# Kernel tuning notes

Hardware: AMD Instinct MI355X
Metric: run time of the kernel (lower is better)

## Reference

```python
import jax, jax.numpy as jnp
import numpy as np

HEADS, POINTS = 8, 4
EPS = 1e-5
BS, C, H, W = 2, 256, 200, 200


def _layernorm(x, g, b):
    m = x.mean(-1, keepdims=True)
    v = ((x - m) ** 2).mean(-1, keepdims=True)
    return (x - m) / jnp.sqrt(v + EPS) * g + b


def _sine_pos(bs, Hh, Ww, num_feats, temperature=10000.0):
    # mmdet SinePositionalEncoding with all-zeros mask: cumsum of ones -> 1..H / 1..W
    y = jnp.arange(1, Hh + 1, dtype=jnp.float32)
    x = jnp.arange(1, Ww + 1, dtype=jnp.float32)
    dim_t = jnp.arange(num_feats, dtype=jnp.float32)
    dim_t = temperature ** (2.0 * jnp.floor(dim_t / 2.0) / num_feats)

    def interleave(p):  # p: [N, num_feats] -> [sin(p0),cos(p1),sin(p2),...]
        return jnp.stack((jnp.sin(p[:, 0::2]), jnp.cos(p[:, 1::2])), axis=-1).reshape(p.shape[0], -1)

    pos_x = interleave(x[:, None] / dim_t)  # [W, nf]
    pos_y = interleave(y[:, None] / dim_t)  # [H, nf]
    pos = jnp.concatenate([
        jnp.broadcast_to(pos_y[:, None, :], (Hh, Ww, num_feats)),
        jnp.broadcast_to(pos_x[None, :, :], (Hh, Ww, num_feats)),
    ], axis=-1)  # [H, W, 2*nf] (channel order matches cat((pos_y,pos_x),dim=1) after flatten/permute)
    return jnp.broadcast_to(pos.reshape(1, Hh * Ww, 2 * num_feats), (bs, Hh * Ww, 2 * num_feats))


def _bilinear_sample(v, x, y):
    # v: [bs, heads, H, W, hd]; x, y: [bs, heads, N] pixel coords (align_corners=False, zero padding)
    bs, nh, Hh, Ww, hd = v.shape
    vf = v.reshape(bs, nh, Hh * Ww, hd)
    x0 = jnp.floor(x)
    y0 = jnp.floor(y)
    wx = x - x0
    wy = y - y0

    def gather(xi, yi):
        valid = (xi >= 0) & (xi < Ww) & (yi >= 0) & (yi < Hh)
        xc = jnp.clip(xi, 0, Ww - 1).astype(jnp.int32)
        yc = jnp.clip(yi, 0, Hh - 1).astype(jnp.int32)
        idx = yc * Ww + xc
        g = jnp.take_along_axis(vf, idx[..., None], axis=2)  # [bs, nh, N, hd]
        return g * valid[..., None].astype(v.dtype)

    out = gather(x0, y0) * ((1 - wx) * (1 - wy))[..., None]
    out = out + gather(x0 + 1, y0) * (wx * (1 - wy))[..., None]
    out = out + gather(x0, y0 + 1) * ((1 - wx) * wy)[..., None]
    out = out + gather(x0 + 1, y0 + 1) * (wx * wy)[..., None]
    return out


def _dfa_layer(out, ref, pos, Hh, Ww, p):
    bs, Lq, Cc = out.shape
    hd = Cc // HEADS
    q = out + pos
    value = out @ p['vp_w'].T + p['vp_b']  # [bs, Lq, C]
    off = (q @ p['off_w'].T + p['off_b']).reshape(bs, Lq, HEADS, POINTS, 2)
    aw = jax.nn.softmax((q @ p['aw_w'].T + p['aw_b']).reshape(bs, Lq, HEADS, POINTS), axis=-1)
    norm = jnp.array([Ww, Hh], dtype=out.dtype)
    loc = ref[None, :, None, None, :] + off / norm  # [bs, Lq, heads, P, 2] normalized [0,1]
    x = loc[..., 0] * Ww - 0.5
    y = loc[..., 1] * Hh - 0.5
    v = value.reshape(bs, Lq, HEADS, hd).transpose(0, 2, 1, 3).reshape(bs, HEADS, Hh, Ww, hd)
    xt = x.transpose(0, 2, 1, 3).reshape(bs, HEADS, Lq * POINTS)
    yt = y.transpose(0, 2, 1, 3).reshape(bs, HEADS, Lq * POINTS)
    samp = _bilinear_sample(v, xt, yt).reshape(bs, HEADS, Lq, POINTS, hd)
    attn = jnp.einsum('bhqpd,bqhp->bqhd', samp, aw).reshape(bs, Lq, Cc)
    attn = attn @ p['op_w'].T + p['op_b']
    out = _layernorm(out + attn, p['ln1_g'], p['ln1_b'])
    ffn = jax.nn.relu(out @ p['l1_w'].T + p['l1_b']) @ p['l2_w'].T + p['l2_b']
    return _layernorm(out + ffn, p['ln2_g'], p['ln2_b'])


def setup_inputs() -> dict:
    key = jax.random.key(0)
    ks = jax.random.split(key, 20)
    s = 0.02
    L = 3
    return {
        'bev_feat': jax.random.normal(ks[0], (BS, C, H, W), jnp.float32),
        'proj_q_w': jax.random.normal(ks[1], (C, C), jnp.float32) * s,
        'proj_q_b': jax.random.normal(ks[2], (C,), jnp.float32) * s,
        'off_w': jax.random.normal(ks[3], (L, HEADS * POINTS * 2, C), jnp.float32) * s,
        'off_b': jax.random.normal(ks[4], (L, HEADS * POINTS * 2), jnp.float32) * s,
        'aw_w': jax.random.normal(ks[5], (L, HEADS * POINTS, C), jnp.float32) * s,
        'aw_b': jax.random.normal(ks[6], (L, HEADS * POINTS), jnp.float32) * s,
        'vp_w': jax.random.normal(ks[7], (L, C, C), jnp.float32) * s,
        'vp_b': jax.random.normal(ks[8], (L, C), jnp.float32) * s,
        'op_w': jax.random.normal(ks[9], (L, C, C), jnp.float32) * s,
        'op_b': jax.random.normal(ks[10], (L, C), jnp.float32) * s,
        'ln1_g': jnp.ones((L, C), jnp.float32),
        'ln1_b': jnp.zeros((L, C), jnp.float32),
        'l1_w': jax.random.normal(ks[11], (L, C, C), jnp.float32) * s,
        'l1_b': jax.random.normal(ks[12], (L, C), jnp.float32) * s,
        'l2_w': jax.random.normal(ks[13], (L, C, C), jnp.float32) * s,
        'l2_b': jax.random.normal(ks[14], (L, C), jnp.float32) * s,
        'ln2_g': jnp.ones((L, C), jnp.float32),
        'ln2_b': jnp.zeros((L, C), jnp.float32),
    }


def reference(bev_feat, proj_q_w, proj_q_b, off_w, off_b, aw_w, aw_b, vp_w, vp_b,
              op_w, op_b, ln1_g, ln1_b, l1_w, l1_b, l2_w, l2_b, ln2_g, ln2_b):
    bs, Cc, Hh, Ww = bev_feat.shape
    x = bev_feat.reshape(bs, Cc, Hh * Ww).transpose(0, 2, 1)  # [bs, HW, C]
    out = x @ proj_q_w.T + proj_q_b
    # reference points: pixel centers normalized to [0,1]
    ry, rx = jnp.meshgrid(jnp.linspace(0.5, Hh - 0.5, Hh) / Hh,
                          jnp.linspace(0.5, Ww - 0.5, Ww) / Ww, indexing='ij')
    ref = jnp.stack([rx.reshape(-1), ry.reshape(-1)], axis=-1).astype(bev_feat.dtype)  # [HW, 2]
    pos = _sine_pos(bs, Hh, Ww, Cc // 2).astype(bev_feat.dtype)
    n_layers = off_w.shape[0]
    for i in range(n_layers):
        p = dict(off_w=off_w[i], off_b=off_b[i], aw_w=aw_w[i], aw_b=aw_b[i],
                 vp_w=vp_w[i], vp_b=vp_b[i], op_w=op_w[i], op_b=op_b[i],
                 ln1_g=ln1_g[i], ln1_b=ln1_b[i], l1_w=l1_w[i], l1_b=l1_b[i],
                 l2_w=l2_w[i], l2_b=l2_b[i], ln2_g=ln2_g[i], ln2_b=ln2_b[i])
        out = _dfa_layer(out, ref, pos, Hh, Ww, p)
    return out.transpose(0, 2, 1).reshape(bs, Cc, Hh, Ww)
```

## Files before the change

### kernel.cpp

```cpp
#include <hip/hip_runtime.h>
#include <math.h>

#define HEADS 8
#define POINTS 4
#define BSZ 2
#define CDIM 256
#define HH 200
#define WW 200
#define LQ (HH * WW)
#define MTOT (BSZ * LQ)
#define NLAYERS 3

typedef __attribute__((ext_vector_type(8))) short shortx8;
typedef __attribute__((ext_vector_type(4))) float floatx4;

__device__ __forceinline__ ushort f2b(float f) {
    union { float f; unsigned u; } v; v.f = f;
    unsigned r = v.u + 0x7fffu + ((v.u >> 16) & 1u);
    return (ushort)(r >> 16);
}
__device__ __forceinline__ float b2f(ushort b) {
    union { unsigned u; float f; } v; v.u = ((unsigned)b) << 16;
    return v.f;
}
__device__ __forceinline__ float bitsf(unsigned u) {
    union { unsigned u; float f; } v; v.u = u;
    return v.f;
}

__global__ __launch_bounds__(256)
void cvt_kernel(const float* __restrict__ in, ushort* __restrict__ out)
{
    const int i = (blockIdx.x * 256 + threadIdx.x) * 4;
    const float4 v = *(const float4*)(in + i);
    ushort4 o;
    o.x = f2b(v.x); o.y = f2b(v.y); o.z = f2b(v.z); o.w = f2b(v.w);
    *(ushort4*)(out + i) = o;
}

__global__ __launch_bounds__(256)
void build_offaw(const float* __restrict__ offw, const float* __restrict__ offb,
                 const float* __restrict__ aww, const float* __restrict__ awb,
                 ushort* __restrict__ wout, float* __restrict__ bout)
{
    const int blk = blockIdx.x;
    const int i = blk >> 7;
    const int r = blk & 127;
    const int c = threadIdx.x;
    float v = 0.f;
    if (r < 64)      v = offw[((size_t)i * 64 + r) * CDIM + c];
    else if (r < 96) v = aww[((size_t)i * 32 + (r - 64)) * CDIM + c];
    wout[((size_t)i * 128 + r) * CDIM + c] = f2b(v);
    if (c == 0) {
        float bb = 0.f;
        if (r < 64)      bb = offb[i * 64 + r];
        else if (r < 96) bb = awb[i * 32 + (r - 64)];
        bout[i * 128 + r] = bb;
    }
}

__global__ __launch_bounds__(256)
void pos_kernel(ushort* __restrict__ pos)
{
    const int idx = blockIdx.x * 256 + threadIdx.x;
    const int c = idx & 255;
    const int l = idx >> 8;
    const int cc = c & 127;
    const float coord = (c < 128) ? (float)(l / WW + 1) : (float)(l % WW + 1);
    const float expo = (float)(2 * (cc >> 1)) * (1.0f / 128.0f);
    const float t = powf(10000.0f, expo);
    const float ph = coord / t;
    pos[idx] = f2b((cc & 1) ? cosf(ph) : sinf(ph));
}

__global__ __launch_bounds__(256)
void bevT_kernel(const float* __restrict__ in, ushort* __restrict__ out)
{
    __shared__ float tile[32][33];
    const int b = blockIdx.z;
    const int l0 = blockIdx.x * 32;
    const int c0 = blockIdx.y * 32;
    const float* ib = in + (size_t)b * CDIM * LQ;
    ushort* ob = out + (size_t)b * LQ * CDIM;
    #pragma unroll
    for (int j = 0; j < 32; j += 8)
        tile[threadIdx.y + j][threadIdx.x] =
            ib[(size_t)(c0 + threadIdx.y + j) * LQ + l0 + threadIdx.x];
    __syncthreads();
    #pragma unroll
    for (int j = 0; j < 32; j += 8)
        ob[(size_t)(l0 + threadIdx.y + j) * CDIM + c0 + threadIdx.x] =
            f2b(tile[threadIdx.x][threadIdx.y + j]);
}

#define LSTR 40

template<bool RELU, bool F32OUT, bool BF16OUT, bool QOUT>
__global__ __launch_bounds__(256)
void mfma_gemm(const ushort* __restrict__ A, const ushort* __restrict__ B,
               const float* __restrict__ bias,
               float* __restrict__ Cf, ushort* __restrict__ Cb,
               ushort* __restrict__ Cq, const ushort* __restrict__ posb,
               int N, int K)
{
    __shared__ ushort As[128 * LSTR];
    __shared__ ushort Bs[128 * LSTR];
    const int tid = threadIdx.x;
    const int lane = tid & 63;
    const int wave = tid >> 6;
    const int wr = (wave >> 1) * 64;
    const int wc = (wave & 1) * 64;
    const int rowBase = blockIdx.y * 128;
    const int colBase = blockIdx.x * 128;

    floatx4 acc[4][4];
    #pragma unroll
    for (int i = 0; i < 4; i++)
        #pragma unroll
        for (int j = 0; j < 4; j++) {
            floatx4 z = {0.f, 0.f, 0.f, 0.f};
            acc[i][j] = z;
        }

    const int strow = tid >> 2;
    const int stcol = (tid & 3) * 8;
    const int kq = (lane >> 4) * 8;
    const int lr = lane & 15;

    for (int k0 = 0; k0 < K; k0 += 32) {
        #pragma unroll
        for (int j = 0; j < 2; j++) {
            const int r = j * 64 + strow;
            const uint4 av = *(const uint4*)(A + (size_t)(rowBase + r) * K + k0 + stcol);
            const uint4 bv = *(const uint4*)(B + (size_t)(colBase + r) * K + k0 + stcol);
            *(uint4*)(As + r * LSTR + stcol) = av;
            *(uint4*)(Bs + r * LSTR + stcol) = bv;
        }
        __syncthreads();
        shortx8 af[4], bf[4];
        #pragma unroll
        for (int t = 0; t < 4; t++) {
            af[t] = *(const shortx8*)(As + (wr + t * 16 + lr) * LSTR + kq);
            bf[t] = *(const shortx8*)(Bs + (wc + t * 16 + lr) * LSTR + kq);
        }
        #pragma unroll
        for (int mt = 0; mt < 4; mt++)
            #pragma unroll
            for (int nt = 0; nt < 4; nt++)
                acc[mt][nt] = __builtin_amdgcn_mfma_f32_16x16x32_bf16(
                    af[mt], bf[nt], acc[mt][nt], 0, 0, 0);
        __syncthreads();
    }

    const int colB = colBase + wc + lr;
    const int rowB = rowBase + wr + (lane >> 4) * 4;
    #pragma unroll
    for (int mt = 0; mt < 4; mt++) {
        #pragma unroll
        for (int r = 0; r < 4; r++) {
            const int m = rowB + mt * 16 + r;
            const int pr = (m >= LQ) ? m - LQ : m;
            #pragma unroll
            for (int nt = 0; nt < 4; nt++) {
                const int n = colB + nt * 16;
                float v = acc[mt][nt][r] + bias[n];
                if (RELU) v = fmaxf(v, 0.f);
                if (F32OUT) Cf[(size_t)m * N + n] = v;
                if (BF16OUT) Cb[(size_t)m * N + n] = f2b(v);
                if (QOUT) {
                    const float pv = b2f(posb[(size_t)pr * CDIM + n]);
                    Cq[(size_t)m * N + n] = f2b(v + pv);
                }
            }
        }
    }
}

__global__ __launch_bounds__(256)
void sample_kernel(const ushort* __restrict__ val,
                   const float* __restrict__ offaw,
                   ushort* __restrict__ attn)
{
    const int wave = threadIdx.x >> 6;
    const int lane = threadIdx.x & 63;
    const int m = blockIdx.x * 4 + wave;
    const int b = (m >= LQ) ? 1 : 0;
    const int l = m - b * LQ;
    const int head = lane >> 3;
    const int c = head * 32 + (lane & 7) * 4;

    const float* row = offaw + (size_t)m * 128;
    const float4 lg  = *(const float4*)(row + 64 + head * 4);
    const float4 o01 = *(const float4*)(row + head * 8);
    const float4 o23 = *(const float4*)(row + head * 8 + 4);

    const float mx = fmaxf(fmaxf(lg.x, lg.y), fmaxf(lg.z, lg.w));
    const float e0 = expf(lg.x - mx), e1 = expf(lg.y - mx);
    const float e2 = expf(lg.z - mx), e3 = expf(lg.w - mx);
    const float inv = 1.0f / (e0 + e1 + e2 + e3);
    const float awv[4] = {e0 * inv, e1 * inv, e2 * inv, e3 * inv};

    const float lx = (float)(l % WW);
    const float ly = (float)(l / WW);
    const float px[4] = {lx + o01.x, lx + o01.z, lx + o23.x, lx + o23.z};
    const float py[4] = {ly + o01.y, ly + o01.w, ly + o23.y, ly + o23.w};

    const ushort* vb = val + (size_t)b * LQ * CDIM;
    uint2 cv[16];
    float cw[16];
    #pragma unroll
    for (int p = 0; p < POINTS; p++) {
        const float x = px[p], y = py[p];
        const float xf = floorf(x), yf = floorf(y);
        const int x0 = (int)xf, y0 = (int)yf;
        const float wx = x - xf, wy = y - yf;
        const int x0c = min(max(x0, 0), WW - 1);
        const int x1c = min(max(x0 + 1, 0), WW - 1);
        const int y0c = min(max(y0, 0), HH - 1);
        const int y1c = min(max(y0 + 1, 0), HH - 1);
        const float vx0 = (x0 >= 0 && x0 < WW) ? 1.f : 0.f;
        const float vx1 = (x0 + 1 >= 0 && x0 + 1 < WW) ? 1.f : 0.f;
        const float vy0 = (y0 >= 0 && y0 < HH) ? 1.f : 0.f;
        const float vy1 = (y0 + 1 >= 0 && y0 + 1 < HH) ? 1.f : 0.f;
        const float a = awv[p];
        cw[p * 4 + 0] = a * (1.f - wx) * (1.f - wy) * vx0 * vy0;
        cw[p * 4 + 1] = a * wx * (1.f - wy) * vx1 * vy0;
        cw[p * 4 + 2] = a * (1.f - wx) * wy * vx0 * vy1;
        cw[p * 4 + 3] = a * wx * wy * vx1 * vy1;
        const int r0 = y0c * WW, r1 = y1c * WW;
        cv[p * 4 + 0] = *(const uint2*)(vb + (size_t)(r0 + x0c) * CDIM + c);
        cv[p * 4 + 1] = *(const uint2*)(vb + (size_t)(r0 + x1c) * CDIM + c);
        cv[p * 4 + 2] = *(const uint2*)(vb + (size_t)(r1 + x0c) * CDIM + c);
        cv[p * 4 + 3] = *(const uint2*)(vb + (size_t)(r1 + x1c) * CDIM + c);
    }
    float a0 = 0.f, a1 = 0.f, a2 = 0.f, a3 = 0.f;
    #pragma unroll
    for (int i = 0; i < 16; i++) {
        const float wgt = cw[i];
        a0 = fmaf(wgt, bitsf(cv[i].x << 16), a0);
        a1 = fmaf(wgt, bitsf(cv[i].x & 0xffff0000u), a1);
        a2 = fmaf(wgt, bitsf(cv[i].y << 16), a2);
        a3 = fmaf(wgt, bitsf(cv[i].y & 0xffff0000u), a3);
    }
    ushort4 o;
    o.x = f2b(a0); o.y = f2b(a1); o.z = f2b(a2); o.w = f2b(a3);
    *(ushort4*)(attn + (size_t)m * CDIM + c) = o;
}

__global__ __launch_bounds__(256)
void ln_kernel(float* __restrict__ io, const ushort* __restrict__ add,
               const float* __restrict__ g, const float* __restrict__ beta,
               ushort* __restrict__ outb, ushort* __restrict__ qout,
               const ushort* __restrict__ posb)
{
    const int row = blockIdx.x * 4 + (threadIdx.x >> 6);
    const int lane = threadIdx.x & 63;
    float4* rp = (float4*)(io + (size_t)row * CDIM);
    float4 x = rp[lane];
    const ushort4 av = *(const ushort4*)(add + (size_t)row * CDIM + lane * 4);
    x.x += b2f(av.x); x.y += b2f(av.y); x.z += b2f(av.z); x.w += b2f(av.w);
    float s = x.x + x.y + x.z + x.w;
    float sq = x.x * x.x + x.y * x.y + x.z * x.z + x.w * x.w;
    #pragma unroll
    for (int o = 32; o >= 1; o >>= 1) {
        s += __shfl_xor(s, o, 64);
        sq += __shfl_xor(sq, o, 64);
    }
    const float mean = s * (1.0f / CDIM);
    const float var = sq * (1.0f / CDIM) - mean * mean;
    const float rstd = rsqrtf(var + 1e-5f);
    const float4 gv = *(const float4*)(g + lane * 4);
    const float4 bv = *(const float4*)(beta + lane * 4);
    float4 o4;
    o4.x = (x.x - mean) * rstd * gv.x + bv.x;
    o4.y = (x.y - mean) * rstd * gv.y + bv.y;
    o4.z = (x.z - mean) * rstd * gv.z + bv.z;
    o4.w = (x.w - mean) * rstd * gv.w + bv.w;
    rp[lane] = o4;
    ushort4 ob;
    ob.x = f2b(o4.x); ob.y = f2b(o4.y); ob.z = f2b(o4.z); ob.w = f2b(o4.w);
    *(ushort4*)(outb + (size_t)row * CDIM + lane * 4) = ob;
    if (qout) {
        const int pr = (row >= LQ) ? row - LQ : row;
        const ushort4 pp = *(const ushort4*)(posb + (size_t)pr * CDIM + lane * 4);
        ushort4 qq;
        qq.x = f2b(o4.x + b2f(pp.x)); qq.y = f2b(o4.y + b2f(pp.y));
        qq.z = f2b(o4.z + b2f(pp.z)); qq.w = f2b(o4.w + b2f(pp.w));
        *(ushort4*)(qout + (size_t)row * CDIM + lane * 4) = qq;
    }
}

__global__ __launch_bounds__(256)
void transpose_out(const float* __restrict__ in, float* __restrict__ outp)
{
    __shared__ float tile[32][33];
    const int b = blockIdx.z;
    const int l0 = blockIdx.x * 32;
    const int c0 = blockIdx.y * 32;
    const float* ib = in + (size_t)b * LQ * CDIM;
    float* ob = outp + (size_t)b * CDIM * LQ;
    #pragma unroll
    for (int j = 0; j < 32; j += 8)
        tile[threadIdx.y + j][threadIdx.x] =
            ib[(size_t)(l0 + threadIdx.y + j) * CDIM + c0 + threadIdx.x];
    __syncthreads();
    #pragma unroll
    for (int j = 0; j < 32; j += 8)
        ob[(size_t)(c0 + threadIdx.y + j) * LQ + l0 + threadIdx.x] =
            tile[threadIdx.x][threadIdx.y + j];
}

extern "C" void kernel_launch(void* const* d_in, const int* in_sizes, int n_in,
                              void* d_out, int out_size, void* d_ws, size_t ws_size,
                              hipStream_t stream)
{
    const float* bev      = (const float*)d_in[0];
    const float* proj_q_w = (const float*)d_in[1];
    const float* proj_q_b = (const float*)d_in[2];
    const float* off_w    = (const float*)d_in[3];
    const float* off_b    = (const float*)d_in[4];
    const float* aw_w     = (const float*)d_in[5];
    const float* aw_b     = (const float*)d_in[6];
    const float* vp_w     = (const float*)d_in[7];
    const float* vp_b     = (const float*)d_in[8];
    const float* op_w     = (const float*)d_in[9];
    const float* op_b     = (const float*)d_in[10];
    const float* ln1_g    = (const float*)d_in[11];
    const float* ln1_b    = (const float*)d_in[12];
    const float* l1_w     = (const float*)d_in[13];
    const float* l1_b     = (const float*)d_in[14];
    const float* l2_w     = (const float*)d_in[15];
    const float* l2_b     = (const float*)d_in[16];
    const float* ln2_g    = (const float*)d_in[17];
    const float* ln2_b    = (const float*)d_in[18];
    float* outp = (float*)d_out;

    char* w = (char*)d_ws;
    float*  out_f   = (float*)(w);
    float*  offaw_f = (float*)(w + 81920000);
    ushort* tmp_b   = (ushort*)(w + 122880000);
    ushort* out_b   = (ushort*)(w + 163840000);
    ushort* q_b     = (ushort*)(w + 204800000);
    ushort* val_b   = (ushort*)(w + 245760000);
    ushort* pos_b   = (ushort*)(w + 286720000);
    ushort* w_b     = (ushort*)(w + 307200000);
    ushort* wproj = w_b;
    ushort* wvp   = w_b + 65536;
    ushort* wop   = w_b + 65536 + 196608;
    ushort* wl1   = w_b + 65536 + 2 * 196608;
    ushort* wl2   = w_b + 65536 + 3 * 196608;
    ushort* wofa  = w_b + 65536 + 4 * 196608;
    float*  bofa  = (float*)(w + 307200000 + 2 * (65536 + 4 * 196608 + 98304));

    const dim3 blk(256);

    cvt_kernel<<<dim3(65536 / 1024), blk, 0, stream>>>(proj_q_w, wproj);
    cvt_kernel<<<dim3(196608 / 1024), blk, 0, stream>>>(vp_w, wvp);
    cvt_kernel<<<dim3(196608 / 1024), blk, 0, stream>>>(op_w, wop);
    cvt_kernel<<<dim3(196608 / 1024), blk, 0, stream>>>(l1_w, wl1);
    cvt_kernel<<<dim3(196608 / 1024), blk, 0, stream>>>(l2_w, wl2);
    build_offaw<<<dim3(3 * 128), blk, 0, stream>>>(off_w, off_b, aw_w, aw_b, wofa, bofa);
    pos_kernel<<<dim3((LQ * CDIM) / 256), blk, 0, stream>>>(pos_b);
    bevT_kernel<<<dim3(LQ / 32, CDIM / 32, BSZ), dim3(32, 8), 0, stream>>>(bev, val_b);

    const dim3 g256(CDIM / 128, MTOT / 128);
    const dim3 g128(1, MTOT / 128);

    mfma_gemm<false, true, true, true><<<g256, blk, 0, stream>>>(
        val_b, wproj, proj_q_b, out_f, out_b, q_b, pos_b, CDIM, CDIM);

    for (int i = 0; i < NLAYERS; i++) {
        mfma_gemm<false, false, true, false><<<g256, blk, 0, stream>>>(
            out_b, wvp + (size_t)i * 65536, vp_b + (size_t)i * CDIM,
            nullptr, val_b, nullptr, nullptr, CDIM, CDIM);
        mfma_gemm<false, true, false, false><<<g128, blk, 0, stream>>>(
            q_b, wofa + (size_t)i * 32768, bofa + (size_t)i * 128,
            offaw_f, nullptr, nullptr, nullptr, 128, CDIM);
        sample_kernel<<<dim3(MTOT / 4), blk, 0, stream>>>(val_b, offaw_f, q_b);
        mfma_gemm<false, false, true, false><<<g256, blk, 0, stream>>>(
            q_b, wop + (size_t)i * 65536, op_b + (size_t)i * CDIM,
            nullptr, tmp_b, nullptr, nullptr, CDIM, CDIM);
        ln_kernel<<<dim3(MTOT / 4), blk, 0, stream>>>(
            out_f, tmp_b, ln1_g + (size_t)i * CDIM, ln1_b + (size_t)i * CDIM,
            out_b, nullptr, pos_b);
        mfma_gemm<true, false, true, false><<<g256, blk, 0, stream>>>(
            out_b, wl1 + (size_t)i * 65536, l1_b + (size_t)i * CDIM,
            nullptr, val_b, nullptr, nullptr, CDIM, CDIM);
        mfma_gemm<false, false, true, false><<<g256, blk, 0, stream>>>(
            val_b, wl2 + (size_t)i * 65536, l2_b + (size_t)i * CDIM,
            nullptr, tmp_b, nullptr, nullptr, CDIM, CDIM);
        ln_kernel<<<dim3(MTOT / 4), blk, 0, stream>>>(
            out_f, tmp_b, ln2_g + (size_t)i * CDIM, ln2_b + (size_t)i * CDIM,
            out_b, q_b, pos_b);
    }

    transpose_out<<<dim3(LQ / 32, CDIM / 32, BSZ), dim3(32, 8), 0, stream>>>(out_f, outp);
}
```

Before: 1.133 ms.

## Fuse residual add and LayerNorm into full-width GEMM epilogue with direct-to-LDS loads

Adds a new GEMM kernel in which each block computes 64 rows across all 256 output columns. That lets the epilogue add the residual, reduce row statistics across waves through shared memory, and apply LayerNorm, and optionally the positional add, in place. This removes the separate ln_kernel launches and the bf16 tmp round-trip through global memory. Operand tiles are now staged with global_load_lds 16-byte direct-to-LDS loads instead of register staging. In exchange, the epilogue's stores are strided per column, which may coalesce poorly, and the tiling changes from 128x128 blocks to 64x256.

```diff
diff --git a/kernel.cpp b/kernel.cpp
--- a/kernel.cpp
+++ b/kernel.cpp
@@ -26,6 +26,12 @@
 __device__ __forceinline__ float bitsf(unsigned u) {
     union { unsigned u; float f; } v; v.u = u;
     return v.f;
+}
+
+__device__ __forceinline__ void gload16(const void* g, void* l) {
+    __builtin_amdgcn_global_load_lds(
+        (const __attribute__((address_space(1))) void*)g,
+        (__attribute__((address_space(3))) void*)l, 16, 0, 0);
 }
 
 __global__ __launch_bounds__(256)
@@ -137,18 +143,18 @@
             *(uint4*)(Bs + r * LSTR + stcol) = bv;
         }
         __syncthreads();
-        shortx8 af[4], bf[4];
+        shortx8 af[4], bfr[4];
         #pragma unroll
         for (int t = 0; t < 4; t++) {
-            af[t] = *(const shortx8*)(As + (wr + t * 16 + lr) * LSTR + kq);
-            bf[t] = *(const shortx8*)(Bs + (wc + t * 16 + lr) * LSTR + kq);
+            af[t]  = *(const shortx8*)(As + (wr + t * 16 + lr) * LSTR + kq);
+            bfr[t] = *(const shortx8*)(Bs + (wc + t * 16 + lr) * LSTR + kq);
         }
         #pragma unroll
         for (int mt = 0; mt < 4; mt++)
             #pragma unroll
             for (int nt = 0; nt < 4; nt++)
                 acc[mt][nt] = __builtin_amdgcn_mfma_f32_16x16x32_bf16(
-                    af[mt], bf[nt], acc[mt][nt], 0, 0, 0);
+                    af[mt], bfr[nt], acc[mt][nt], 0, 0, 0);
         __syncthreads();
     }
 
@@ -170,6 +176,145 @@
                 if (QOUT) {
                     const float pv = b2f(posb[(size_t)pr * CDIM + n]);
                     Cq[(size_t)m * N + n] = f2b(v + pv);
+                }
+            }
+        }
+    }
+}
+
+template<bool RELU, bool LN, bool F32OUT, bool BF16OUT, bool QOUT>
+__global__ __launch_bounds__(256)
+void gemm_fused(const ushort* __restrict__ A, const ushort* __restrict__ B,
+                const float* __restrict__ bias,
+                float* __restrict__ resid, ushort* __restrict__ Cb,
+                ushort* __restrict__ Cq, const ushort* __restrict__ posb,
+                const float* __restrict__ g, const float* __restrict__ beta)
+{
+    __shared__ ushort As[64 * 32];
+    __shared__ ushort Bs[256 * 32];
+    __shared__ float2 red[64][4];
+
+    const int tid = threadIdx.x;
+    const int lane = tid & 63;
+    const int wave = tid >> 6;
+    const int lr = lane & 15;
+    const int hi = lane >> 4;
+    const int rowBase = blockIdx.x * 64;
+    const int wc = wave * 64;
+
+    floatx4 acc[4][4];
+    #pragma unroll
+    for (int i = 0; i < 4; i++)
+        #pragma unroll
+        for (int j = 0; j < 4; j++) {
+            floatx4 z = {0.f, 0.f, 0.f, 0.f};
+            acc[i][j] = z;
+        }
+
+    const int srow = lane >> 2;
+    const int scol = (lane & 3) * 8;
+    const ushort* ag = A + (size_t)(rowBase + wave * 16 + srow) * CDIM + scol;
+    const ushort* bg = B + (size_t)(wave * 64 + srow) * CDIM + scol;
+    ushort* al = As + wave * 16 * 32;
+    ushort* bl = Bs + wave * 64 * 32;
+
+    for (int kt = 0; kt < 8; ++kt) {
+        const int ko = kt * 32;
+        gload16(ag + ko, al);
+        gload16(bg + ko, bl);
+        gload16(bg + ko + 16 * CDIM, bl + 16 * 32);
+        gload16(bg + ko + 32 * CDIM, bl + 32 * 32);
+        gload16(bg + ko + 48 * CDIM, bl + 48 * 32);
+        __syncthreads();
+        shortx8 af[4], bfr[4];
+        #pragma unroll
+        for (int t = 0; t < 4; t++) {
+            af[t]  = *(const shortx8*)(As + (t * 16 + lr) * 32 + hi * 8);
+            bfr[t] = *(const shortx8*)(Bs + (wc + t * 16 + lr) * 32 + hi * 8);
+        }
+        #pragma unroll
+        for (int mt = 0; mt < 4; mt++)
+            #pragma unroll
+            for (int nt = 0; nt < 4; nt++)
+                acc[mt][nt] = __builtin_amdgcn_mfma_f32_16x16x32_bf16(
+                    af[mt], bfr[nt], acc[mt][nt], 0, 0, 0);
+        __syncthreads();
+    }
+
+    float bcol[4];
+    #pragma unroll
+    for (int nt = 0; nt < 4; nt++) bcol[nt] = bias[wc + nt * 16 + lr];
+
+    if (LN) {
+        #pragma unroll
+        for (int mt = 0; mt < 4; mt++) {
+            #pragma unroll
+            for (int r = 0; r < 4; r++) {
+                const int mrel = mt * 16 + hi * 4 + r;
+                const float* rrow = resid + (size_t)(rowBase + mrel) * CDIM + wc + lr;
+                float s = 0.f, sq = 0.f;
+                #pragma unroll
+                for (int nt = 0; nt < 4; nt++) {
+                    float x = acc[mt][nt][r] + bcol[nt] + rrow[nt * 16];
+                    acc[mt][nt][r] = x;
+                    s += x; sq += x * x;
+                }
+                #pragma unroll
+                for (int o = 8; o >= 1; o >>= 1) {
+                    s  += __shfl_xor(s, o, 64);
+                    sq += __shfl_xor(sq, o, 64);
+                }
+                if (lr == 0) { float2 t2; t2.x = s; t2.y = sq; red[mrel][wave] = t2; }
+            }
+        }
+        __syncthreads();
+        float gcol[4], btcol[4];
+        #pragma unroll
+        for (int nt = 0; nt < 4; nt++) {
+            gcol[nt]  = g[wc + nt * 16 + lr];
+            btcol[nt] = beta[wc + nt * 16 + lr];
+        }
+        #pragma unroll
+        for (int mt = 0; mt < 4; mt++) {
+            #pragma unroll
+            for (int r = 0; r < 4; r++) {
+                const int mrel = mt * 16 + hi * 4 + r;
+                const int m = rowBase + mrel;
+                const float2 t0 = red[mrel][0], t1 = red[mrel][1];
+                const float2 t2 = red[mrel][2], t3 = red[mrel][3];
+                const float S  = (t0.x + t1.x) + (t2.x + t3.x);
+                const float SQ = (t0.y + t1.y) + (t2.y + t3.y);
+                const float mean = S * (1.0f / CDIM);
+                const float var = SQ * (1.0f / CDIM) - mean * mean;
+                const float rstd = rsqrtf(var + 1e-5f);
+                const int pr = (m >= LQ) ? m - LQ : m;
+                #pragma unroll
+                for (int nt = 0; nt < 4; nt++) {
+                    const int col = wc + nt * 16 + lr;
+                    const float y = (acc[mt][nt][r] - mean) * rstd * gcol[nt] + btcol[nt];
+                    resid[(size_t)m * CDIM + col] = y;
+                    if (BF16OUT) Cb[(size_t)m * CDIM + col] = f2b(y);
+                    if (QOUT) Cq[(size_t)m * CDIM + col] =
+                        f2b(y + b2f(posb[(size_t)pr * CDIM + col]));
+                }
+            }
+        }
+    } else {
+        #pragma unroll
+        for (int mt = 0; mt < 4; mt++) {
+            #pragma unroll
+            for (int r = 0; r < 4; r++) {
+                const int m = rowBase + mt * 16 + hi * 4 + r;
+                const int pr = (m >= LQ) ? m - LQ : m;
+                #pragma unroll
+                for (int nt = 0; nt < 4; nt++) {
+                    const int col = wc + nt * 16 + lr;
+                    float y = acc[mt][nt][r] + bcol[nt];
+                    if (RELU) y = fmaxf(y, 0.f);
+                    if (F32OUT) resid[(size_t)m * CDIM + col] = y;
+                    if (BF16OUT) Cb[(size_t)m * CDIM + col] = f2b(y);
+                    if (QOUT) Cq[(size_t)m * CDIM + col] =
+                        f2b(y + b2f(posb[(size_t)pr * CDIM + col]));
                 }
             }
         }
@@ -248,49 +393,6 @@
 }
 
 __global__ __launch_bounds__(256)
-void ln_kernel(float* __restrict__ io, const ushort* __restrict__ add,
-               const float* __restrict__ g, const float* __restrict__ beta,
-               ushort* __restrict__ outb, ushort* __restrict__ qout,
-               const ushort* __restrict__ posb)
-{
-    const int row = blockIdx.x * 4 + (threadIdx.x >> 6);
-    const int lane = threadIdx.x & 63;
-    float4* rp = (float4*)(io + (size_t)row * CDIM);
-    float4 x = rp[lane];
-    const ushort4 av = *(const ushort4*)(add + (size_t)row * CDIM + lane * 4);
-    x.x += b2f(av.x); x.y += b2f(av.y); x.z += b2f(av.z); x.w += b2f(av.w);
-    float s = x.x + x.y + x.z + x.w;
-    float sq = x.x * x.x + x.y * x.y + x.z * x.z + x.w * x.w;
-    #pragma unroll
-    for (int o = 32; o >= 1; o >>= 1) {
-        s += __shfl_xor(s, o, 64);
-        sq += __shfl_xor(sq, o, 64);
-    }
-    const float mean = s * (1.0f / CDIM);
-    const float var = sq * (1.0f / CDIM) - mean * mean;
-    const float rstd = rsqrtf(var + 1e-5f);
-    const float4 gv = *(const float4*)(g + lane * 4);
-    const float4 bv = *(const float4*)(beta + lane * 4);
-    float4 o4;
-    o4.x = (x.x - mean) * rstd * gv.x + bv.x;
-    o4.y = (x.y - mean) * rstd * gv.y + bv.y;
-    o4.z = (x.z - mean) * rstd * gv.z + bv.z;
-    o4.w = (x.w - mean) * rstd * gv.w + bv.w;
-    rp[lane] = o4;
-    ushort4 ob;
-    ob.x = f2b(o4.x); ob.y = f2b(o4.y); ob.z = f2b(o4.z); ob.w = f2b(o4.w);
-    *(ushort4*)(outb + (size_t)row * CDIM + lane * 4) = ob;
-    if (qout) {
-        const int pr = (row >= LQ) ? row - LQ : row;
-        const ushort4 pp = *(const ushort4*)(posb + (size_t)pr * CDIM + lane * 4);
-        ushort4 qq;
-        qq.x = f2b(o4.x + b2f(pp.x)); qq.y = f2b(o4.y + b2f(pp.y));
-        qq.z = f2b(o4.z + b2f(pp.z)); qq.w = f2b(o4.w + b2f(pp.w));
-        *(ushort4*)(qout + (size_t)row * CDIM + lane * 4) = qq;
-    }
-}
-
-__global__ __launch_bounds__(256)
 void transpose_out(const float* __restrict__ in, float* __restrict__ outp)
 {
     __shared__ float tile[32][33];
@@ -338,7 +440,6 @@
     char* w = (char*)d_ws;
     float*  out_f   = (float*)(w);
     float*  offaw_f = (float*)(w + 81920000);
-    ushort* tmp_b   = (ushort*)(w + 122880000);
     ushort* out_b   = (ushort*)(w + 163840000);
     ushort* q_b     = (ushort*)(w + 204800000);
     ushort* val_b   = (ushort*)(w + 245760000);
@@ -363,35 +464,31 @@
     pos_kernel<<<dim3((LQ * CDIM) / 256), blk, 0, stream>>>(pos_b);
     bevT_kernel<<<dim3(LQ / 32, CDIM / 32, BSZ), dim3(32, 8), 0, stream>>>(bev, val_b);
 
-    const dim3 g256(CDIM / 128, MTOT / 128);
+    const dim3 gF(MTOT / 64);
     const dim3 g128(1, MTOT / 128);
 
-    mfma_gemm<false, true, true, true><<<g256, blk, 0, stream>>>(
-        val_b, wproj, proj_q_b, out_f, out_b, q_b, pos_b, CDIM, CDIM);
+    gemm_fused<false, false, true, true, true><<<gF, blk, 0, stream>>>(
+        val_b, wproj, proj_q_b, out_f, out_b, q_b, pos_b, nullptr, nullptr);
 
     for (int i = 0; i < NLAYERS; i++) {
-        mfma_gemm<false, false, true, false><<<g256, blk, 0, stream>>>(
+        gemm_fused<false, false, false, true, false><<<gF, blk, 0, stream>>>(
             out_b, wvp + (size_t)i * 65536, vp_b + (size_t)i * CDIM,
-            nullptr, val_b, nullptr, nullptr, CDIM, CDIM);
+            nullptr, val_b, nullptr, nullptr, nullptr, nullptr);
         mfma_gemm<false, true, false, false><<<g128, blk, 0, stream>>>(
             q_b, wofa + (size_t)i * 32768, bofa + (size_t)i * 128,
             offaw_f, nullptr, nullptr, nullptr, 128, CDIM);
         sample_kernel<<<dim3(MTOT / 4), blk, 0, stream>>>(val_b, offaw_f, q_b);
-        mfma_gemm<false, false, true, false><<<g256, blk, 0, stream>>>(
+        gemm_fused<false, true, false, true, false><<<gF, blk, 0, stream>>>(
             q_b, wop + (size_t)i * 65536, op_b + (size_t)i * CDIM,
-            nullptr, tmp_b, nullptr, nullptr, CDIM, CDIM);
-        ln_kernel<<<dim3(MTOT / 4), blk, 0, stream>>>(
-            out_f, tmp_b, ln1_g + (size_t)i * CDIM, ln1_b + (size_t)i * CDIM,
-            out_b, nullptr, pos_b);
-        mfma_gemm<true, false, true, false><<<g256, blk, 0, stream>>>(
+            out_f, out_b, nullptr, pos_b,
+            ln1_g + (size_t)i * CDIM, ln1_b + (size_t)i * CDIM);
+        gemm_fused<true, false, false, true, false><<<gF, blk, 0, stream>>>(
             out_b, wl1 + (size_t)i * 65536, l1_b + (size_t)i * CDIM,
-            nullptr, val_b, nullptr, nullptr, CDIM, CDIM);
-        mfma_gemm<false, false, true, false><<<g256, blk, 0, stream>>>(
+            nullptr, val_b, nullptr, nullptr, nullptr, nullptr);
+        gemm_fused<false, true, false, true, true><<<gF, blk, 0, stream>>>(
             val_b, wl2 + (size_t)i * 65536, l2_b + (size_t)i * CDIM,
-            nullptr, tmp_b, nullptr, nullptr, CDIM, CDIM);
-        ln_kernel<<<dim3(MTOT / 4), blk, 0, stream>>>(
-            out_f, tmp_b, ln2_g + (size_t)i * CDIM, ln2_b + (size_t)i * CDIM,
-            out_b, q_b, pos_b);
+            out_f, out_b, q_b, pos_b,
+            ln2_g + (size_t)i * CDIM, ln2_b + (size_t)i * CDIM);
     }
 
     transpose_out<<<dim3(LQ / 32, CDIM / 32, BSZ), dim3(32, 8), 0, stream>>>(out_f, outp);
```

Measured after the change: 1.089 ms. 1.04x faster.
